# Kernel tuning notes

Measured on AMD Instinct MI355X. Metric: run time of the kernel, lower is better.

Reference implementation:

```python
import jax, jax.numpy as jnp
import numpy as np
import math

HIDDEN = 1024
N_HEADS = 16
HEAD_DIM = HIDDEN // N_HEADS

def _safe(x, clamp_val):
    x = jnp.nan_to_num(x, nan=0.0, posinf=0.0, neginf=0.0)
    return jnp.clip(x, -clamp_val, clamp_val)

def _stable_linear(x, W, b):
    # StableLinear: clamp(50) -> linear -> clamp(50)
    x = _safe(x, 50.0)
    out = x @ W.T + b
    return _safe(out, 50.0)

def setup_inputs() -> dict:
    key = jax.random.key(0)
    ks = jax.random.split(key, 12)
    bsz, q_len, kv_len = 4, 1024, 2048
    q = jax.random.normal(ks[0], (bsz, q_len, HIDDEN), dtype=jnp.float32)
    kv = jax.random.normal(ks[1], (bsz, kv_len, HIDDEN), dtype=jnp.float32)
    key_padding_mask = jax.random.bernoulli(ks[2], 0.1, (bsz, kv_len))
    bound = 1.0 / math.sqrt(HIDDEN)
    def mk_w(k):
        return jax.random.uniform(k, (HIDDEN, HIDDEN), jnp.float32, -bound, bound)
    def mk_b(k):
        return jax.random.uniform(k, (HIDDEN,), jnp.float32, -bound, bound)
    return {
        'q': q, 'kv': kv, 'key_padding_mask': key_padding_mask,
        'Wq': mk_w(ks[3]), 'bq': mk_b(ks[4]),
        'Wk': mk_w(ks[5]), 'bk': mk_b(ks[6]),
        'Wv': mk_w(ks[7]), 'bv': mk_b(ks[8]),
        'Wo': mk_w(ks[9]), 'bo': mk_b(ks[10]),
    }

def reference(q, kv, key_padding_mask, Wq, bq, Wk, bk, Wv, bv, Wo, bo):
    bsz, q_len, _ = q.shape
    kv_len = kv.shape[1]
    # outer _safe(50) then StableLinear's own _safe(50) (idempotent)
    qh = _stable_linear(_safe(q, 50.0), Wq, bq)
    kh = _stable_linear(_safe(kv, 50.0), Wk, bk)
    vh = _stable_linear(_safe(kv, 50.0), Wv, bv)
    # [b, h, s, d]
    qh = qh.reshape(bsz, q_len, N_HEADS, HEAD_DIM).transpose(0, 2, 1, 3)
    kh = kh.reshape(bsz, kv_len, N_HEADS, HEAD_DIM).transpose(0, 2, 1, 3)
    vh = vh.reshape(bsz, kv_len, N_HEADS, HEAD_DIM).transpose(0, 2, 1, 3)
    scores = jnp.einsum('bhqd,bhkd->bhqk', qh.astype(jnp.float32), kh.astype(jnp.float32))
    scores = scores / math.sqrt(HEAD_DIM)
    scores = jnp.clip(scores, -80.0, 80.0)
    scores = jnp.where(key_padding_mask[:, None, None, :], -10000.0, scores)
    attn = jax.nn.softmax(scores, axis=-1)  # dropout is identity in eval mode
    out = jnp.einsum('bhqk,bhkd->bhqd', attn, vh.astype(jnp.float32))
    out = out.transpose(0, 2, 1, 3).reshape(bsz, q_len, HIDDEN)
    out = _stable_linear(_safe(out, 50.0), Wo, bo)
    return _safe(out, 50.0)
```

## Files before the change

kernel.cpp:

```cpp
#include <hip/hip_runtime.h>
#include <hip/hip_bf16.h>
#include <stdint.h>
#include <math.h>

#define HIDDEN 1024
#define NHEADS 16
#define HDIM   64
#define BSZ    4
#define QLEN   1024
#define KVLEN  2048

typedef __bf16 bf16_t;
typedef __bf16 bf16x8 __attribute__((ext_vector_type(8)));
typedef __bf16 bf16x4 __attribute__((ext_vector_type(4)));
typedef float  f32x4  __attribute__((ext_vector_type(4)));

#define C_SCALE 0.18033688f
#define C_FMADD (-43.2808512f)

#define GLOAD16(g, l) \
    __builtin_amdgcn_global_load_lds((const __attribute__((address_space(1))) void*)(g), \
                                     (__attribute__((address_space(3))) void*)(l), 16, 0, 0)

__device__ __forceinline__ float clamp50(float v) {
    return fminf(fmaxf(v, -50.f), 50.f);
}

__global__ void mask_prep_kernel(const void* __restrict__ raw, float* __restrict__ maskadd) {
    __shared__ int s_float, s_multi;
    const int t = threadIdx.x;
    if (t == 0) { s_float = 0; s_multi = 0; }
    __syncthreads();
    const uint32_t* w = (const uint32_t*)raw;
    int cf = 0, cm = 0;
    for (int i = t; i < 2048; i += blockDim.x) {
        uint32_t v = w[i];
        if (v == 0x3F800000u) cf++;
        else if (v & 0xFFFFFF00u) cm++;
    }
    if (cf) atomicAdd(&s_float, cf);
    if (cm) atomicAdd(&s_multi, cm);
    __syncthreads();
    const int mode = (s_float > 0) ? 2 : ((s_multi > 0) ? 0 : 1);
    const int base = blockIdx.x * 512;
    for (int i = base + t; i < base + 512; i += blockDim.x) {
        bool m;
        if (mode == 2)      m = ((const float*)raw)[i] != 0.0f;
        else if (mode == 1) m = ((const int*)raw)[i] != 0;
        else                m = ((const unsigned char*)raw)[i] != 0;
        maskadd[i] = m ? (-100000.0f + C_FMADD) : C_FMADD;
    }
}

#define NQ4  ((BSZ * QLEN  * HIDDEN) / 4)
#define NKV4 ((BSZ * KVLEN * HIDDEN) / 4)
#define NW4  ((HIDDEN * HIDDEN) / 4)

__global__ void cvt_all_kernel(const float* __restrict__ q, const float* __restrict__ kv,
                               const float* __restrict__ W0, const float* __restrict__ W1,
                               const float* __restrict__ W2, const float* __restrict__ W3,
                               bf16_t* __restrict__ q_bf, bf16_t* __restrict__ kv_bf,
                               bf16_t* __restrict__ w_bf) {
    const int i = blockIdx.x * blockDim.x + threadIdx.x;
    const float4* src;
    bf16x4* dst;
    if (i < NQ4) {
        src = (const float4*)q + i;            dst = (bf16x4*)q_bf + i;
    } else if (i < NQ4 + NKV4) {
        const int j = i - NQ4;
        src = (const float4*)kv + j;           dst = (bf16x4*)kv_bf + j;
    } else {
        const int j = i - (NQ4 + NKV4);
        const int ws = j >> 18, off = j & (NW4 - 1);
        const float* W = (ws == 0) ? W0 : (ws == 1) ? W1 : (ws == 2) ? W2 : W3;
        src = (const float4*)W + off;          dst = (bf16x4*)w_bf + (size_t)ws * NW4 + off;
    }
    const float4 v = *src;
    bf16x4 o;
    o[0] = (bf16_t)clamp50(v.x); o[1] = (bf16_t)clamp50(v.y);
    o[2] = (bf16_t)clamp50(v.z); o[3] = (bf16_t)clamp50(v.w);
    *dst = o;
}

template <int NT>
__device__ __forceinline__ void gemm_core(const char* __restrict__ Ab, const char* __restrict__ Bb,
                                          bf16_t* Als, bf16_t* Bls,
                                          f32x4 (&acc)[4][NT / 32],
                                          int wave, int lane, int wm, int wn)
{
    constexpr int NF = NT / 32;
    const int srcsw = ((lane & 7) ^ (lane >> 3)) << 4;
    const int rowl = lane >> 3;

    for (int kt = 0; kt < HIDDEN / 64; ++kt) {
#pragma unroll
        for (int i = 0; i < 4; ++i) {
            const int row = i * 32 + wave * 8 + rowl;
            GLOAD16(Ab + (size_t)row * (HIDDEN * 2) + kt * 128 + srcsw,
                    (char*)Als + i * 4096 + wave * 1024);
        }
#pragma unroll
        for (int i = 0; i < NF; ++i) {
            const int row = i * 32 + wave * 8 + rowl;
            GLOAD16(Bb + (size_t)row * (HIDDEN * 2) + kt * 128 + srcsw,
                    (char*)Bls + i * 4096 + wave * 1024);
        }
        __syncthreads();
#pragma unroll
        for (int kc = 0; kc < 2; ++kc) {
            const int kbyte = kc * 64 + ((lane >> 4) << 4);
            bf16x8 af[4], bfr[NF];
#pragma unroll
            for (int f2 = 0; f2 < 4; ++f2) {
                const int arow = wm * 64 + f2 * 16 + (lane & 15);
                af[f2] = *(const bf16x8*)((const char*)Als + arow * 128 + (kbyte ^ ((arow & 7) << 4)));
            }
#pragma unroll
            for (int f2 = 0; f2 < NF; ++f2) {
                const int brow = wn * (NT / 2) + f2 * 16 + (lane & 15);
                bfr[f2] = *(const bf16x8*)((const char*)Bls + brow * 128 + (kbyte ^ ((brow & 7) << 4)));
            }
#pragma unroll
            for (int mf = 0; mf < 4; ++mf)
#pragma unroll
                for (int nf = 0; nf < NF; ++nf)
                    acc[mf][nf] = __builtin_amdgcn_mfma_f32_16x16x32_bf16(af[mf], bfr[nf], acc[mf][nf], 0, 0, 0);
        }
        __syncthreads();
    }
}

template <int NF>
__device__ __forceinline__ void epi_head(f32x4 (&acc)[4][NF], const float* bias,
                                         bf16_t* out, int m0, int n0, int slog,
                                         int wm, int wn, int lane)
{
#pragma unroll
    for (int mf = 0; mf < 4; ++mf) {
#pragma unroll
        for (int nf = 0; nf < NF; ++nf) {
            const int gn = n0 + wn * (NF * 16) + nf * 16 + (lane & 15);
            const float bv = bias[gn];
#pragma unroll
            for (int r = 0; r < 4; ++r) {
                const int gm = m0 + wm * 64 + mf * 16 + ((lane >> 4) << 2) + r;
                const float v = clamp50(acc[mf][nf][r] + bv);
                const int b = gm >> slog;
                const int s = gm & ((1 << slog) - 1);
                const int h = gn >> 6, d = gn & 63;
                out[((((size_t)(b * NHEADS + h)) << slog) + s) * HDIM + d] = (bf16_t)v;
            }
        }
    }
}

template <int EPI, int NT>
__global__ __launch_bounds__(256)
void gemm_bt_kernel(const bf16_t* __restrict__ A, const bf16_t* __restrict__ B,
                    const float* __restrict__ bias, void* __restrict__ out, int slog)
{
    constexpr int NF = NT / 32;
    __shared__ __align__(16) bf16_t Smem[(128 + NT) * 64];
    bf16_t* Als = Smem;
    bf16_t* Bls = Smem + 128 * 64;

    const int m0 = blockIdx.y * 128;
    const int n0 = blockIdx.x * NT;
    const int t = threadIdx.x;
    const int wave = t >> 6, lane = t & 63;
    const int wm = wave >> 1, wn = wave & 1;

    f32x4 acc[4][NF] = {};
    gemm_core<NT>((const char*)A + (size_t)m0 * (HIDDEN * 2),
                  (const char*)B + (size_t)n0 * (HIDDEN * 2),
                  Als, Bls, acc, wave, lane, wm, wn);

    if (EPI == 0) {
        epi_head<NF>(acc, bias, (bf16_t*)out, m0, n0, slog, wm, wn, lane);
    } else {
#pragma unroll
        for (int mf = 0; mf < 4; ++mf) {
#pragma unroll
            for (int nf = 0; nf < NF; ++nf) {
                const int gn = n0 + wn * (NF * 16) + nf * 16 + (lane & 15);
                const float bv = bias[gn];
#pragma unroll
                for (int r = 0; r < 4; ++r) {
                    const int gm = m0 + wm * 64 + mf * 16 + ((lane >> 4) << 2) + r;
                    ((float*)out)[(size_t)gm * HIDDEN + gn] = clamp50(acc[mf][nf][r] + bv);
                }
            }
        }
    }
}

__global__ __launch_bounds__(256)
void gemm_kv_fused(const bf16_t* __restrict__ A, const bf16_t* __restrict__ Bk,
                   const bf16_t* __restrict__ Bv, const float* __restrict__ bk,
                   const float* __restrict__ bv, bf16_t* __restrict__ kh,
                   bf16_t* __restrict__ vt)
{
    __shared__ __align__(16) bf16_t Smem[2 * 128 * 64];
    bf16_t* Als = Smem;
    bf16_t* Bls = Smem + 128 * 64;

    const int isV = blockIdx.x >> 3;
    const int n0 = (blockIdx.x & 7) * 128;
    const int m0 = blockIdx.y * 128;
    const int t = threadIdx.x;
    const int wave = t >> 6, lane = t & 63;
    const int wm = wave >> 1, wn = wave & 1;
    const bf16_t* B = isV ? Bv : Bk;
    const float* bias = isV ? bv : bk;

    f32x4 acc[4][4] = {};
    gemm_core<128>((const char*)A + (size_t)m0 * (HIDDEN * 2),
                   (const char*)B + (size_t)n0 * (HIDDEN * 2),
                   Als, Bls, acc, wave, lane, wm, wn);

    if (!isV) {
        epi_head<4>(acc, bias, kh, m0, n0, 11, wm, wn, lane);
        return;
    }

    bf16_t* Cls = Smem;
    const int dl = t >> 1;
    const int sh = (t & 1) << 5;
    const int gn = n0 + dl;
    const int h = gn >> 6, d = gn & 63;
    const int bb = m0 >> 11;
    bf16_t* dst = vt + ((size_t)((bb * NHEADS + h) * HDIM + d)) * KVLEN
                + (m0 & (KVLEN - 1)) + sh;
#pragma unroll
    for (int ph = 0; ph < 2; ++ph) {
        if (wm == ph) {
#pragma unroll
            for (int mf = 0; mf < 4; ++mf) {
#pragma unroll
                for (int nf = 0; nf < 4; ++nf) {
                    const int dcol = wn * 64 + nf * 16 + (lane & 15);
                    const float bv2 = bias[n0 + dcol];
#pragma unroll
                    for (int r = 0; r < 4; ++r) {
                        const int srow = mf * 16 + ((lane >> 4) << 2) + r;
                        Cls[srow * 130 + dcol] = (bf16_t)clamp50(acc[mf][nf][r] + bv2);
                    }
                }
            }
        }
        __syncthreads();
#pragma unroll
        for (int j0 = 0; j0 < 32; j0 += 8) {
            bf16x8 v;
#pragma unroll
            for (int j = 0; j < 8; ++j) v[j] = Cls[(sh + j0 + j) * 130 + dl];
            *(bf16x8*)(dst + ph * 64 + j0) = v;
        }
        __syncthreads();
    }
}

__global__ __launch_bounds__(256)
void attn_fwd_kernel(const bf16_t* __restrict__ Qh, const bf16_t* __restrict__ Kh,
                     const bf16_t* __restrict__ Vt, const float* __restrict__ maskadd,
                     bf16_t* __restrict__ aout)
{
    __shared__ __align__(16) bf16_t Kls[2][64 * 64];
    __shared__ __align__(16) bf16_t Vls[2][64 * 64];

    const int f = blockIdx.x;
    const int o = (f & 7) * 64 + (f >> 3);
    const int qt = o & 7;
    const int bh = o >> 3;
    const int b = bh >> 4, h = bh & 15;
    const int t = threadIdx.x, wave = t >> 6, lane = t & 63;
    const int g = lane >> 4;
    const int ql = lane & 15;

    const int qbase = qt * 128 + wave * 32;
    bf16x8 qf[2][2];
#pragma unroll
    for (int qq = 0; qq < 2; ++qq) {
        const bf16_t* qp = Qh + ((size_t)bh * QLEN + qbase + qq * 16 + ql) * HDIM + (g << 3);
        qf[qq][0] = *(const bf16x8*)qp;
        qf[qq][1] = *(const bf16x8*)(qp + 32);
    }

    f32x4 oacc[2][4] = {};
    float lsum[2] = {0.f, 0.f};

    const int srcsw = ((lane & 7) ^ (lane >> 3)) << 4;
    const int R0 = wave * 8 + (lane >> 3);
    const int R1 = R0 + 32;
    const int kap0 = 32 * (R0 >> 5) + 8 * ((R0 >> 2) & 3) + 4 * ((R0 >> 4) & 1) + (R0 & 3);
    const int kap1 = 32 * (R1 >> 5) + 8 * ((R1 >> 2) & 3) + 4 * ((R1 >> 4) & 1) + (R1 & 3);

    const char* Kb = (const char*)(Kh + (size_t)bh * KVLEN * HDIM);
    const char* Vb = (const char*)(Vt + (size_t)bh * HDIM * KVLEN);
    const float* mrow = maskadd + b * KVLEN;
    const int m8g = g * 8;

    GLOAD16(Kb + (size_t)kap0 * 128 + srcsw, (char*)&Kls[0][0] + wave * 1024);
    GLOAD16(Kb + (size_t)kap1 * 128 + srcsw, (char*)&Kls[0][0] + 4096 + wave * 1024);
    GLOAD16(Vb + (size_t)R0 * (KVLEN * 2) + srcsw, (char*)&Vls[0][0] + wave * 1024);
    GLOAD16(Vb + (size_t)R1 * (KVLEN * 2) + srcsw, (char*)&Vls[0][0] + 4096 + wave * 1024);

    f32x4 madd_c[4], madd_n[4];
    madd_c[0] = *(const f32x4*)(mrow + m8g);
    madd_c[1] = *(const f32x4*)(mrow + m8g + 4);
    madd_c[2] = *(const f32x4*)(mrow + m8g + 32);
    madd_c[3] = *(const f32x4*)(mrow + m8g + 36);
    __syncthreads();

    for (int kt = 0; kt < KVLEN / 64; ++kt) {
        const int cur = kt & 1;
        if (kt < KVLEN / 64 - 1) {
            const size_t ko = (size_t)(kt + 1) * 8192;
            GLOAD16(Kb + ko + (size_t)kap0 * 128 + srcsw,
                    (char*)&Kls[cur ^ 1][0] + wave * 1024);
            GLOAD16(Kb + ko + (size_t)kap1 * 128 + srcsw,
                    (char*)&Kls[cur ^ 1][0] + 4096 + wave * 1024);
            GLOAD16(Vb + (size_t)R0 * (KVLEN * 2) + (size_t)(kt + 1) * 128 + srcsw,
                    (char*)&Vls[cur ^ 1][0] + wave * 1024);
            GLOAD16(Vb + (size_t)R1 * (KVLEN * 2) + (size_t)(kt + 1) * 128 + srcsw,
                    (char*)&Vls[cur ^ 1][0] + 4096 + wave * 1024);
            const float* mn = mrow + (kt + 1) * 64 + m8g;
            madd_n[0] = *(const f32x4*)(mn);
            madd_n[1] = *(const f32x4*)(mn + 4);
            madd_n[2] = *(const f32x4*)(mn + 32);
            madd_n[3] = *(const f32x4*)(mn + 36);
        }
        const char* Kc = (const char*)&Kls[cur][0];
        const char* Vc = (const char*)&Vls[cur][0];

        f32x4 sacc[2][4] = {};
#pragma unroll
        for (int kb = 0; kb < 4; ++kb) {
            const int key = kb * 16 + ql;
            const int rowoff = key * 128;
            const int sw = (key & 7) << 4;
            const int kb0 = g << 4;
            const bf16x8 kf0 = *(const bf16x8*)(Kc + rowoff + ((kb0)      ^ sw));
            const bf16x8 kf1 = *(const bf16x8*)(Kc + rowoff + ((kb0 + 64) ^ sw));
#pragma unroll
            for (int qq = 0; qq < 2; ++qq) {
                sacc[qq][kb] = __builtin_amdgcn_mfma_f32_16x16x32_bf16(kf0, qf[qq][0], sacc[qq][kb], 0, 0, 0);
                sacc[qq][kb] = __builtin_amdgcn_mfma_f32_16x16x32_bf16(kf1, qf[qq][1], sacc[qq][kb], 0, 0, 0);
            }
        }

        bf16x8 pa[2][2];
#pragma unroll
        for (int qq = 0; qq < 2; ++qq) {
            float pv[4][4];
            float ls = 0.f;
#pragma unroll
            for (int kb = 0; kb < 4; ++kb) {
#pragma unroll
                for (int r = 0; r < 4; ++r) {
                    pv[kb][r] = __builtin_amdgcn_exp2f(
                        __builtin_fmaf(sacc[qq][kb][r], C_SCALE, madd_c[kb][r]));
                    ls += pv[kb][r];
                }
            }
            lsum[qq] += ls;
#pragma unroll
            for (int r = 0; r < 4; ++r) {
                pa[qq][0][r]     = (bf16_t)pv[0][r];
                pa[qq][0][4 + r] = (bf16_t)pv[1][r];
                pa[qq][1][r]     = (bf16_t)pv[2][r];
                pa[qq][1][4 + r] = (bf16_t)pv[3][r];
            }
        }

#pragma unroll
        for (int db = 0; db < 4; ++db) {
            const int vrow = db * 16 + ql;
            const int vsw = (vrow & 7) << 4;
            const int kb0 = g << 4;
            const bf16x8 vf0 = *(const bf16x8*)(Vc + vrow * 128 + ((kb0)      ^ vsw));
            const bf16x8 vf1 = *(const bf16x8*)(Vc + vrow * 128 + ((kb0 + 64) ^ vsw));
#pragma unroll
            for (int qq = 0; qq < 2; ++qq) {
                oacc[qq][db] = __builtin_amdgcn_mfma_f32_16x16x32_bf16(pa[qq][0], vf0, oacc[qq][db], 0, 0, 0);
                oacc[qq][db] = __builtin_amdgcn_mfma_f32_16x16x32_bf16(pa[qq][1], vf1, oacc[qq][db], 0, 0, 0);
            }
        }

        __syncthreads();
#pragma unroll
        for (int kb = 0; kb < 4; ++kb) madd_c[kb] = madd_n[kb];
    }

#pragma unroll
    for (int qq = 0; qq < 2; ++qq) {
        float l = lsum[qq];
        l += __shfl_xor(l, 16);
        l += __shfl_xor(l, 32);
        lsum[qq] = l;
    }
    const int rbase = g << 2;
#pragma unroll
    for (int qq = 0; qq < 2; ++qq) {
#pragma unroll
        for (int r = 0; r < 4; ++r) {
            const float Lr = __shfl(lsum[qq], rbase + r);
            const float inv = 1.0f / Lr;
            const int qrow = qbase + qq * 16 + rbase + r;
            bf16_t* orow = aout + ((size_t)(b * QLEN + qrow)) * HIDDEN + h * HDIM;
#pragma unroll
            for (int db = 0; db < 4; ++db)
                orow[db * 16 + ql] = (bf16_t)(oacc[qq][db][r] * inv);
        }
    }
}

extern "C" void kernel_launch(void* const* d_in, const int* in_sizes, int n_in,
                              void* d_out, int out_size, void* d_ws, size_t ws_size,
                              hipStream_t stream) {
    (void)in_sizes; (void)n_in; (void)out_size; (void)ws_size;
    const float* q   = (const float*)d_in[0];
    const float* kv  = (const float*)d_in[1];
    const void*  msk = d_in[2];
    const float* Wq  = (const float*)d_in[3];
    const float* bq  = (const float*)d_in[4];
    const float* Wk  = (const float*)d_in[5];
    const float* bk  = (const float*)d_in[6];
    const float* Wv  = (const float*)d_in[7];
    const float* bv  = (const float*)d_in[8];
    const float* Wo  = (const float*)d_in[9];
    const float* bo  = (const float*)d_in[10];

    char* ws = (char*)d_ws;
    const size_t MB = 1024 * 1024;
    float*  maskadd = (float*)ws;
    bf16_t* w_bf  = (bf16_t*)(ws + 32 * 1024);
    bf16_t* q_bf  = (bf16_t*)(ws + 32 * 1024 + 8  * MB);
    bf16_t* kv_bf = (bf16_t*)(ws + 32 * 1024 + 16 * MB);
    bf16_t* qh    = (bf16_t*)(ws + 32 * 1024 + 32 * MB);
    bf16_t* kh    = (bf16_t*)(ws + 32 * 1024 + 40 * MB);
    bf16_t* vt    = (bf16_t*)(ws + 32 * 1024 + 56 * MB);
    bf16_t* aout  = q_bf;

    bf16_t* wq_bf = w_bf;
    bf16_t* wk_bf = w_bf + (size_t)HIDDEN * HIDDEN;
    bf16_t* wv_bf = w_bf + (size_t)2 * HIDDEN * HIDDEN;
    bf16_t* wo_bf = w_bf + (size_t)3 * HIDDEN * HIDDEN;

    mask_prep_kernel<<<dim3(16), 256, 0, stream>>>(msk, maskadd);
    cvt_all_kernel<<<dim3((NQ4 + NKV4 + 4 * NW4) / 256), 256, 0, stream>>>(
        q, kv, Wq, Wk, Wv, Wo, q_bf, kv_bf, w_bf);

    gemm_bt_kernel<0, 64><<<dim3(16, 32), 256, 0, stream>>>(q_bf, wq_bf, bq, qh, 10);
    gemm_kv_fused<<<dim3(16, 64), 256, 0, stream>>>(kv_bf, wk_bf, wv_bf, bk, bv, kh, vt);

    attn_fwd_kernel<<<dim3(512), 256, 0, stream>>>(qh, kh, vt, maskadd, aout);

    gemm_bt_kernel<1, 64><<<dim3(16, 32), 256, 0, stream>>>(aout, wo_bf, bo, d_out, 10);
}
```

Baseline: 167.0 us.

## Split attention key tiles across two wave groups and fold mask prep into convert

The attention kernel now runs 512 threads per block. Each query-wave pair splits every 64-key tile into two 32-key halves, and the partial outputs and row sums are reduced through shared memory at the end. This doubles the waves per block to hide latency, at the cost of an extra shared-memory reduction and a larger LDS footprint. The mask preparation kernel is also merged into the conversion kernel as four extra blocks, which removes one launch.

```diff
diff --git a/kernel.cpp b/kernel.cpp
--- a/kernel.cpp
+++ b/kernel.cpp
@@ -26,41 +26,43 @@
     return fminf(fmaxf(v, -50.f), 50.f);
 }
 
-__global__ void mask_prep_kernel(const void* __restrict__ raw, float* __restrict__ maskadd) {
-    __shared__ int s_float, s_multi;
-    const int t = threadIdx.x;
-    if (t == 0) { s_float = 0; s_multi = 0; }
-    __syncthreads();
-    const uint32_t* w = (const uint32_t*)raw;
-    int cf = 0, cm = 0;
-    for (int i = t; i < 2048; i += blockDim.x) {
-        uint32_t v = w[i];
-        if (v == 0x3F800000u) cf++;
-        else if (v & 0xFFFFFF00u) cm++;
-    }
-    if (cf) atomicAdd(&s_float, cf);
-    if (cm) atomicAdd(&s_multi, cm);
-    __syncthreads();
-    const int mode = (s_float > 0) ? 2 : ((s_multi > 0) ? 0 : 1);
-    const int base = blockIdx.x * 512;
-    for (int i = base + t; i < base + 512; i += blockDim.x) {
-        bool m;
-        if (mode == 2)      m = ((const float*)raw)[i] != 0.0f;
-        else if (mode == 1) m = ((const int*)raw)[i] != 0;
-        else                m = ((const unsigned char*)raw)[i] != 0;
-        maskadd[i] = m ? (-100000.0f + C_FMADD) : C_FMADD;
-    }
-}
-
 #define NQ4  ((BSZ * QLEN  * HIDDEN) / 4)
 #define NKV4 ((BSZ * KVLEN * HIDDEN) / 4)
 #define NW4  ((HIDDEN * HIDDEN) / 4)
+#define NCVT ((NQ4 + NKV4 + 4 * NW4) / 256)
 
 __global__ void cvt_all_kernel(const float* __restrict__ q, const float* __restrict__ kv,
                                const float* __restrict__ W0, const float* __restrict__ W1,
                                const float* __restrict__ W2, const float* __restrict__ W3,
                                bf16_t* __restrict__ q_bf, bf16_t* __restrict__ kv_bf,
-                               bf16_t* __restrict__ w_bf) {
+                               bf16_t* __restrict__ w_bf,
+                               const void* __restrict__ msk, float* __restrict__ maskadd) {
+    if (blockIdx.x >= NCVT) {
+        __shared__ int s_float, s_multi;
+        const int t = threadIdx.x;
+        if (t == 0) { s_float = 0; s_multi = 0; }
+        __syncthreads();
+        const uint32_t* w = (const uint32_t*)msk;
+        int cf = 0, cm = 0;
+        for (int i = t; i < 2048; i += 256) {
+            uint32_t v = w[i];
+            if (v == 0x3F800000u) cf++;
+            else if (v & 0xFFFFFF00u) cm++;
+        }
+        if (cf) atomicAdd(&s_float, cf);
+        if (cm) atomicAdd(&s_multi, cm);
+        __syncthreads();
+        const int mode = (s_float > 0) ? 2 : ((s_multi > 0) ? 0 : 1);
+        const int base = (blockIdx.x - NCVT) * 2048;
+        for (int i = base + t; i < base + 2048; i += 256) {
+            bool m;
+            if (mode == 2)      m = ((const float*)msk)[i] != 0.0f;
+            else if (mode == 1) m = ((const int*)msk)[i] != 0;
+            else                m = ((const unsigned char*)msk)[i] != 0;
+            maskadd[i] = m ? (-100000.0f + C_FMADD) : C_FMADD;
+        }
+        return;
+    }
     const int i = blockIdx.x * blockDim.x + threadIdx.x;
     const float4* src;
     bf16x4* dst;
@@ -260,13 +262,15 @@
     }
 }
 
-__global__ __launch_bounds__(256)
+__global__ __launch_bounds__(512)
 void attn_fwd_kernel(const bf16_t* __restrict__ Qh, const bf16_t* __restrict__ Kh,
                      const bf16_t* __restrict__ Vt, const float* __restrict__ maskadd,
                      bf16_t* __restrict__ aout)
 {
     __shared__ __align__(16) bf16_t Kls[2][64 * 64];
     __shared__ __align__(16) bf16_t Vls[2][64 * 64];
+    __shared__ __align__(16) float Cbuf[4][32 * 64];
+    __shared__ float Lbuf[4][2][16];
 
     const int f = blockIdx.x;
     const int o = (f & 7) * 64 + (f >> 3);
@@ -274,10 +278,11 @@
     const int bh = o >> 3;
     const int b = bh >> 4, h = bh & 15;
     const int t = threadIdx.x, wave = t >> 6, lane = t & 63;
-    const int g = lane >> 4;
-    const int ql = lane & 15;
-
-    const int qbase = qt * 128 + wave * 32;
+    const int wq = wave & 3;
+    const int wg = wave >> 2;
+    const int g = lane >> 4, ql = lane & 15;
+
+    const int qbase = qt * 128 + wq * 32;
     bf16x8 qf[2][2];
 #pragma unroll
     for (int qq = 0; qq < 2; ++qq) {
@@ -290,56 +295,42 @@
     float lsum[2] = {0.f, 0.f};
 
     const int srcsw = ((lane & 7) ^ (lane >> 3)) << 4;
-    const int R0 = wave * 8 + (lane >> 3);
-    const int R1 = R0 + 32;
-    const int kap0 = 32 * (R0 >> 5) + 8 * ((R0 >> 2) & 3) + 4 * ((R0 >> 4) & 1) + (R0 & 3);
-    const int kap1 = 32 * (R1 >> 5) + 8 * ((R1 >> 2) & 3) + 4 * ((R1 >> 4) & 1) + (R1 & 3);
+    const int R = wave * 8 + (lane >> 3);
+    const int kap = 32 * (R >> 5) + 8 * ((R >> 2) & 3) + 4 * ((R >> 4) & 1) + (R & 3);
 
     const char* Kb = (const char*)(Kh + (size_t)bh * KVLEN * HDIM);
     const char* Vb = (const char*)(Vt + (size_t)bh * HDIM * KVLEN);
-    const float* mrow = maskadd + b * KVLEN;
-    const int m8g = g * 8;
-
-    GLOAD16(Kb + (size_t)kap0 * 128 + srcsw, (char*)&Kls[0][0] + wave * 1024);
-    GLOAD16(Kb + (size_t)kap1 * 128 + srcsw, (char*)&Kls[0][0] + 4096 + wave * 1024);
-    GLOAD16(Vb + (size_t)R0 * (KVLEN * 2) + srcsw, (char*)&Vls[0][0] + wave * 1024);
-    GLOAD16(Vb + (size_t)R1 * (KVLEN * 2) + srcsw, (char*)&Vls[0][0] + 4096 + wave * 1024);
-
-    f32x4 madd_c[4], madd_n[4];
-    madd_c[0] = *(const f32x4*)(mrow + m8g);
-    madd_c[1] = *(const f32x4*)(mrow + m8g + 4);
-    madd_c[2] = *(const f32x4*)(mrow + m8g + 32);
-    madd_c[3] = *(const f32x4*)(mrow + m8g + 36);
+    const float* mrow = maskadd + b * KVLEN + wg * 32 + g * 8;
+    const int kb0 = g << 4;
+    const int vcol = wg * 64 + kb0;
+
+    GLOAD16(Kb + (size_t)kap * 128 + srcsw, (char*)&Kls[0][0] + wave * 1024);
+    GLOAD16(Vb + (size_t)R * (KVLEN * 2) + srcsw, (char*)&Vls[0][0] + wave * 1024);
+    f32x4 madd_c[2], madd_n[2];
+    madd_c[0] = *(const f32x4*)(mrow);
+    madd_c[1] = *(const f32x4*)(mrow + 4);
     __syncthreads();
 
     for (int kt = 0; kt < KVLEN / 64; ++kt) {
         const int cur = kt & 1;
         if (kt < KVLEN / 64 - 1) {
             const size_t ko = (size_t)(kt + 1) * 8192;
-            GLOAD16(Kb + ko + (size_t)kap0 * 128 + srcsw,
+            GLOAD16(Kb + ko + (size_t)kap * 128 + srcsw,
                     (char*)&Kls[cur ^ 1][0] + wave * 1024);
-            GLOAD16(Kb + ko + (size_t)kap1 * 128 + srcsw,
-                    (char*)&Kls[cur ^ 1][0] + 4096 + wave * 1024);
-            GLOAD16(Vb + (size_t)R0 * (KVLEN * 2) + (size_t)(kt + 1) * 128 + srcsw,
+            GLOAD16(Vb + (size_t)R * (KVLEN * 2) + (size_t)(kt + 1) * 128 + srcsw,
                     (char*)&Vls[cur ^ 1][0] + wave * 1024);
-            GLOAD16(Vb + (size_t)R1 * (KVLEN * 2) + (size_t)(kt + 1) * 128 + srcsw,
-                    (char*)&Vls[cur ^ 1][0] + 4096 + wave * 1024);
-            const float* mn = mrow + (kt + 1) * 64 + m8g;
-            madd_n[0] = *(const f32x4*)(mn);
-            madd_n[1] = *(const f32x4*)(mn + 4);
-            madd_n[2] = *(const f32x4*)(mn + 32);
-            madd_n[3] = *(const f32x4*)(mn + 36);
+            madd_n[0] = *(const f32x4*)(mrow + (kt + 1) * 64);
+            madd_n[1] = *(const f32x4*)(mrow + (kt + 1) * 64 + 4);
         }
         const char* Kc = (const char*)&Kls[cur][0];
         const char* Vc = (const char*)&Vls[cur][0];
 
-        f32x4 sacc[2][4] = {};
-#pragma unroll
-        for (int kb = 0; kb < 4; ++kb) {
-            const int key = kb * 16 + ql;
+        f32x4 sacc[2][2] = {};
+#pragma unroll
+        for (int kb = 0; kb < 2; ++kb) {
+            const int key = wg * 32 + kb * 16 + ql;
             const int rowoff = key * 128;
             const int sw = (key & 7) << 4;
-            const int kb0 = g << 4;
             const bf16x8 kf0 = *(const bf16x8*)(Kc + rowoff + ((kb0)      ^ sw));
             const bf16x8 kf1 = *(const bf16x8*)(Kc + rowoff + ((kb0 + 64) ^ sw));
 #pragma unroll
@@ -349,13 +340,13 @@
             }
         }
 
-        bf16x8 pa[2][2];
+        bf16x8 pa[2];
 #pragma unroll
         for (int qq = 0; qq < 2; ++qq) {
-            float pv[4][4];
+            float pv[2][4];
             float ls = 0.f;
 #pragma unroll
-            for (int kb = 0; kb < 4; ++kb) {
+            for (int kb = 0; kb < 2; ++kb) {
 #pragma unroll
                 for (int r = 0; r < 4; ++r) {
                     pv[kb][r] = __builtin_amdgcn_exp2f(
@@ -366,10 +357,8 @@
             lsum[qq] += ls;
 #pragma unroll
             for (int r = 0; r < 4; ++r) {
-                pa[qq][0][r]     = (bf16_t)pv[0][r];
-                pa[qq][0][4 + r] = (bf16_t)pv[1][r];
-                pa[qq][1][r]     = (bf16_t)pv[2][r];
-                pa[qq][1][4 + r] = (bf16_t)pv[3][r];
+                pa[qq][r]     = (bf16_t)pv[0][r];
+                pa[qq][4 + r] = (bf16_t)pv[1][r];
             }
         }
 
@@ -377,19 +366,15 @@
         for (int db = 0; db < 4; ++db) {
             const int vrow = db * 16 + ql;
             const int vsw = (vrow & 7) << 4;
-            const int kb0 = g << 4;
-            const bf16x8 vf0 = *(const bf16x8*)(Vc + vrow * 128 + ((kb0)      ^ vsw));
-            const bf16x8 vf1 = *(const bf16x8*)(Vc + vrow * 128 + ((kb0 + 64) ^ vsw));
-#pragma unroll
-            for (int qq = 0; qq < 2; ++qq) {
-                oacc[qq][db] = __builtin_amdgcn_mfma_f32_16x16x32_bf16(pa[qq][0], vf0, oacc[qq][db], 0, 0, 0);
-                oacc[qq][db] = __builtin_amdgcn_mfma_f32_16x16x32_bf16(pa[qq][1], vf1, oacc[qq][db], 0, 0, 0);
-            }
-        }
-
-        __syncthreads();
-#pragma unroll
-        for (int kb = 0; kb < 4; ++kb) madd_c[kb] = madd_n[kb];
+            const bf16x8 vf = *(const bf16x8*)(Vc + vrow * 128 + (vcol ^ vsw));
+#pragma unroll
+            for (int qq = 0; qq < 2; ++qq)
+                oacc[qq][db] = __builtin_amdgcn_mfma_f32_16x16x32_bf16(pa[qq], vf, oacc[qq][db], 0, 0, 0);
+        }
+
+        __syncthreads();
+#pragma unroll
+        for (int kb = 0; kb < 2; ++kb) madd_c[kb] = madd_n[kb];
     }
 
 #pragma unroll
@@ -400,17 +385,34 @@
         lsum[qq] = l;
     }
     const int rbase = g << 2;
-#pragma unroll
-    for (int qq = 0; qq < 2; ++qq) {
-#pragma unroll
-        for (int r = 0; r < 4; ++r) {
-            const float Lr = __shfl(lsum[qq], rbase + r);
-            const float inv = 1.0f / Lr;
-            const int qrow = qbase + qq * 16 + rbase + r;
-            bf16_t* orow = aout + ((size_t)(b * QLEN + qrow)) * HIDDEN + h * HDIM;
+    if (wg == 1) {
+#pragma unroll
+        for (int qq = 0; qq < 2; ++qq) {
 #pragma unroll
             for (int db = 0; db < 4; ++db)
-                orow[db * 16 + ql] = (bf16_t)(oacc[qq][db][r] * inv);
+#pragma unroll
+                for (int r = 0; r < 4; ++r)
+                    Cbuf[wq][(qq * 16 + rbase + r) * 64 + db * 16 + ql] = oacc[qq][db][r];
+            if (lane < 16) Lbuf[wq][qq][lane] = lsum[qq];
+        }
+    }
+    __syncthreads();
+    if (wg == 0) {
+#pragma unroll
+        for (int qq = 0; qq < 2; ++qq) {
+            const float Lq = lsum[qq] + Lbuf[wq][qq][ql];
+#pragma unroll
+            for (int r = 0; r < 4; ++r) {
+                const float Lr = __shfl(Lq, rbase + r);
+                const float inv = 1.0f / Lr;
+                const int qrow = qbase + qq * 16 + rbase + r;
+                bf16_t* orow = aout + ((size_t)(b * QLEN + qrow)) * HIDDEN + h * HDIM;
+#pragma unroll
+                for (int db = 0; db < 4; ++db) {
+                    const float add = Cbuf[wq][(qq * 16 + rbase + r) * 64 + db * 16 + ql];
+                    orow[db * 16 + ql] = (bf16_t)((oacc[qq][db][r] + add) * inv);
+                }
+            }
         }
     }
 }
@@ -447,14 +449,13 @@
     bf16_t* wv_bf = w_bf + (size_t)2 * HIDDEN * HIDDEN;
     bf16_t* wo_bf = w_bf + (size_t)3 * HIDDEN * HIDDEN;
 
-    mask_prep_kernel<<<dim3(16), 256, 0, stream>>>(msk, maskadd);
-    cvt_all_kernel<<<dim3((NQ4 + NKV4 + 4 * NW4) / 256), 256, 0, stream>>>(
-        q, kv, Wq, Wk, Wv, Wo, q_bf, kv_bf, w_bf);
+    cvt_all_kernel<<<dim3(NCVT + 4), 256, 0, stream>>>(
+        q, kv, Wq, Wk, Wv, Wo, q_bf, kv_bf, w_bf, msk, maskadd);
 
     gemm_bt_kernel<0, 64><<<dim3(16, 32), 256, 0, stream>>>(q_bf, wq_bf, bq, qh, 10);
     gemm_kv_fused<<<dim3(16, 64), 256, 0, stream>>>(kv_bf, wk_bf, wv_bf, bk, bv, kh, vt);
 
-    attn_fwd_kernel<<<dim3(512), 256, 0, stream>>>(qh, kh, vt, maskadd, aout);
+    attn_fwd_kernel<<<dim3(512), 512, 0, stream>>>(qh, kh, vt, maskadd, aout);
 
     gemm_bt_kernel<1, 64><<<dim3(16, 32), 256, 0, stream>>>(aout, wo_bf, bo, d_out, 10);
 }
```

Result: faster. 155.7 us (-6.7%).
